# Kernel optimization log

Hardware: AMD Instinct MI355X
Metric: run time of the kernel (lower is better)

## Reference

```python
import jax, jax.numpy as jnp
import numpy as np

B, N, F_IN, ENC = 512, 512, 6, 128
EPS = 1e-5  # BatchNorm1d default eps


def _masked_bn_relu(h, m, gamma, beta):
    # h: [B,N,C]; m: [B,N,1] float mask. BN stats over valid points only,
    # matching torch's first_mlp(x[mask]) gather semantics (biased variance).
    cnt = jnp.maximum(m.sum(), 1.0)
    mean = (h * m).sum(axis=(0, 1)) / cnt
    var = (jnp.square(h - mean) * m).sum(axis=(0, 1)) / cnt
    hn = (h - mean) * jax.lax.rsqrt(var + EPS) * gamma + beta
    return jax.nn.relu(hn)


def setup_inputs() -> dict:
    key = jax.random.key(0)
    ks = jax.random.split(key, 16)
    s = lambda fan_in: 1.0 / np.sqrt(fan_in)
    inp = {
        "x": jax.random.normal(ks[0], (B, N, F_IN), dtype=jnp.float32),
        "mask": jax.random.bernoulli(ks[1], 0.7, (B, N)),
        # first_mlp: Linear(F_IN,128), BN(128), ReLU, Linear(128,256)
        "W1": jax.random.uniform(ks[2], (F_IN, 128), jnp.float32, -s(F_IN), s(F_IN)),
        "b1": jnp.zeros((128,), jnp.float32),
        "g1": jnp.ones((128,), jnp.float32),
        "be1": jnp.zeros((128,), jnp.float32),
        "W2": jax.random.uniform(ks[3], (128, 256), jnp.float32, -s(128), s(128)),
        "b2": jnp.zeros((256,), jnp.float32),
        # second_mlp: Linear(512,256), BN(256), ReLU, Linear(256,ENC)
        "W3": jax.random.uniform(ks[4], (512, 256), jnp.float32, -s(512), s(512)),
        "b3": jnp.zeros((256,), jnp.float32),
        "g2": jnp.ones((256,), jnp.float32),
        "be2": jnp.zeros((256,), jnp.float32),
        "W4": jax.random.uniform(ks[5], (256, ENC), jnp.float32, -s(256), s(256)),
        "b4": jnp.zeros((ENC,), jnp.float32),
    }
    return inp


def reference(x, mask, W1, b1, g1, be1, W2, b2, W3, b3, g2, be2, W4, b4):
    m = mask[..., None].astype(x.dtype)  # [B,N,1]
    # first_mlp on valid points; invalid positions become zeros (scatter into zeros buffer)
    h = x @ W1 + b1
    h = _masked_bn_relu(h, m, g1, be1)
    h = (h @ W2 + b2) * m  # [B,N,256], zeros where mask is False
    pooled = h.max(axis=1)  # [B,256] (zeros participate, as in torch)
    feat = jnp.concatenate(
        [h, jnp.broadcast_to(pooled[:, None, :], (h.shape[0], h.shape[1], pooled.shape[-1]))],
        axis=-1,
    )  # [B,N,512]
    h2 = feat @ W3 + b3
    h2 = _masked_bn_relu(h2, m, g2, be2)
    h2 = (h2 @ W4 + b4) * m  # [B,N,ENC], zeros where invalid
    return h2.max(axis=1)  # [B,ENC]
```

## Files before the change

kernel.cpp:

```cpp
#include <hip/hip_runtime.h>
#include <stdint.h>

#define BB   512
#define NN   512
#define MROWS (BB*NN)
#define RT   (MROWS/64)
#define EPSV 1e-5f

typedef unsigned short u16;
typedef __attribute__((ext_vector_type(8))) short bf16x8;
typedef __attribute__((ext_vector_type(4))) float f32x4;

__device__ __forceinline__ float read_mask(const void* mp, int r, int mode) {
  if (mode == 0) return ((const unsigned char*)mp)[r] ? 1.f : 0.f;
  if (mode == 1) return ((const unsigned int*)mp)[r] ? 1.f : 0.f;
  return ((const unsigned long long*)mp)[r] ? 1.f : 0.f;
}

__device__ __forceinline__ u16 f2bf(float f) {
  union { float f; unsigned int u; } v; v.f = f;
  unsigned int u = v.u;
  return (u16)((u + 0x7FFFu + ((u >> 16) & 1u)) >> 16);
}

__device__ __forceinline__ float bf2f(u16 b) {
  union { unsigned int u; float f; } t;
  t.u = ((unsigned int)b) << 16;
  return t.f;
}

__device__ __forceinline__ unsigned int cvt_pk_bf16(float lo, float hi) {
  unsigned int r;
  asm("v_cvt_pk_bf16_f32 %0, %1, %2" : "=v"(r) : "v"(lo), "v"(hi));
  return r;
}

__global__ __launch_bounds__(256) void k_prep(
    const float* __restrict__ W2, const float* __restrict__ W3, const float* __restrict__ W4,
    const float* __restrict__ b2, const unsigned char* __restrict__ mu,
    u16* __restrict__ w2t, u16* __restrict__ w4t,
    u16* __restrict__ w23t, float* __restrict__ c23, int* __restrict__ mode) {
  __shared__ float row[256];
  __shared__ int c1s, c4s;
  const int blk = blockIdx.x;
  if (blk < 256) {
    const int idx = blk*256 + threadIdx.x;
    if (idx < 32768) {
      const int n = idx >> 7, k = idx & 127;
      w2t[idx] = f2bf(W2[(size_t)k*256 + n]);
    } else {
      const int j = idx - 32768;
      const int n = j >> 8, k = j & 255;
      w4t[j] = f2bf(W4[(size_t)k*128 + n]);
    }
  } else if (blk < 385) {
    const int n = threadIdx.x;
    const int k = blk - 256;
    if (k < 128) {
      row[n] = W2[(size_t)k*256 + n];
      __syncthreads();
      float a0 = 0.f, a1 = 0.f, a2v = 0.f, a3 = 0.f;
      for (int j = 0; j < 256; j += 4) {
        a0 = fmaf(row[j  ], W3[(size_t)(j    )*256 + n], a0);
        a1 = fmaf(row[j+1], W3[(size_t)(j + 1)*256 + n], a1);
        a2v= fmaf(row[j+2], W3[(size_t)(j + 2)*256 + n], a2v);
        a3 = fmaf(row[j+3], W3[(size_t)(j + 3)*256 + n], a3);
      }
      w23t[(size_t)n*128 + k] = f2bf(((a0 + a1) + (a2v + a3)));
    } else {
      float a0 = 0.f, a1 = 0.f, a2v = 0.f, a3 = 0.f;
      for (int j = 0; j < 256; j += 4) {
        a0 = fmaf(b2[j  ], W3[(size_t)(j    )*256 + n], a0);
        a1 = fmaf(b2[j+1], W3[(size_t)(j + 1)*256 + n], a1);
        a2v= fmaf(b2[j+2], W3[(size_t)(j + 2)*256 + n], a2v);
        a3 = fmaf(b2[j+3], W3[(size_t)(j + 3)*256 + n], a3);
      }
      c23[n] = ((a0 + a1) + (a2v + a3));
    }
  } else {
    if (threadIdx.x == 0) { c1s = 0; c4s = 0; }
    __syncthreads();
    for (int i = threadIdx.x; i < 4096; i += 256) {
      const unsigned char b = mu[i];
      if (b) {
        if ((i & 3) == 1) atomicAdd(&c1s, 1);
        if ((i & 7) == 4) atomicAdd(&c4s, 1);
      }
    }
    __syncthreads();
    if (threadIdx.x == 0) *mode = c1s ? 0 : (c4s ? 1 : 2);
  }
}

__global__ __launch_bounds__(256) void k_stats1(
    const float* __restrict__ x, const void* __restrict__ mask,
    const int* __restrict__ modep,
    float* __restrict__ part, float* __restrict__ cntbf) {
  const int mode = *modep;
  const int tid = threadIdx.x;
  const int blk = blockIdx.x;
  float sx[6] = {0,0,0,0,0,0};
  float sxx[21] = {0};
  float cntq[4] = {0,0,0,0};
#pragma unroll
  for (int it = 0; it < 8; ++it) {
    const int r = blk*2048 + it*256 + tid;
    const float mv = read_mask(mask, r, mode);
    const float* xr = x + (size_t)r*6;
    const float2 p0 = *(const float2*)(xr);
    const float2 p1 = *(const float2*)(xr + 2);
    const float2 p2 = *(const float2*)(xr + 4);
    float v[6] = {p0.x, p0.y, p1.x, p1.y, p2.x, p2.y};
    cntq[it >> 1] += mv;
    int idx = 0;
#pragma unroll
    for (int j = 0; j < 6; ++j) {
      sx[j] = fmaf(mv, v[j], sx[j]);
      const float mj = mv * v[j];
#pragma unroll
      for (int k = j; k < 6; ++k) { sxx[idx] = fmaf(mj, v[k], sxx[idx]); ++idx; }
    }
  }
  float vals[32];
#pragma unroll
  for (int j = 0; j < 6; ++j) vals[j] = sx[j];
#pragma unroll
  for (int j = 0; j < 21; ++j) vals[6 + j] = sxx[j];
  vals[27] = 0.f;
#pragma unroll
  for (int q = 0; q < 4; ++q) vals[28 + q] = cntq[q];
#pragma unroll
  for (int j = 0; j < 32; ++j) {
#pragma unroll
    for (int m = 1; m <= 32; m <<= 1)
      vals[j] += __shfl_xor(vals[j], m, 64);
  }
  __shared__ float red[4][32];
  const int wave = tid >> 6, lane = tid & 63;
  if (lane == 0) {
#pragma unroll
    for (int j = 0; j < 32; ++j) red[wave][j] = vals[j];
  }
  __syncthreads();
  if (tid < 32) {
    const float tot = red[0][tid] + red[1][tid] + red[2][tid] + red[3][tid];
    part[(size_t)blk*32 + tid] = tot;
    if (tid >= 28) cntbf[blk*4 + (tid - 28)] = tot;
  }
}

__global__ __launch_bounds__(128) void k_fin1(
    const float* __restrict__ part,
    const float* __restrict__ W1, const float* __restrict__ b1,
    const float* __restrict__ g1, const float* __restrict__ be1,
    float* __restrict__ w1p, float* __restrict__ c1p, float* __restrict__ cntf) {
  __shared__ float tot[32];
  const int t = threadIdx.x;
  if (t < 32) {
    float a0 = 0.f, a1 = 0.f, a2v = 0.f, a3 = 0.f;
    for (int i = 0; i < 128; i += 4) {
      a0 += part[(size_t)(i    )*32 + t];
      a1 += part[(size_t)(i + 1)*32 + t];
      a2v+= part[(size_t)(i + 2)*32 + t];
      a3 += part[(size_t)(i + 3)*32 + t];
    }
    tot[t] = (a0 + a1) + (a2v + a3);
  }
  __syncthreads();
  float cnt = tot[28] + tot[29] + tot[30] + tot[31];
  if (cnt < 1.f) cnt = 1.f;
  if (t == 0) *cntf = cnt;
  const int c = t;
  float w[6];
#pragma unroll
  for (int k = 0; k < 6; ++k) w[k] = W1[k*128 + c];
  float s1 = 0.f;
#pragma unroll
  for (int k = 0; k < 6; ++k) s1 = fmaf(w[k], tot[k], s1);
  s1 /= cnt;
  float q = 0.f;
  {
    int idx = 6;
#pragma unroll
    for (int j = 0; j < 6; ++j) {
      q = fmaf(w[j]*w[j], tot[idx], q); ++idx;
#pragma unroll
      for (int k = j + 1; k < 6; ++k) { q = fmaf(2.f*w[j]*w[k], tot[idx], q); ++idx; }
    }
  }
  float var = q / cnt - s1*s1; if (var < 0.f) var = 0.f;
  const float mean = b1[c] + s1;
  const float a = g1[c] * rsqrtf(var + EPSV);
  const float sh = be1[c] - mean*a;
  c1p[c] = fmaf(b1[c], a, sh - b1[c]*a + (mean - s1)*0.f);
  c1p[c] = fmaf(b1[c], a, be1[c] - mean*a);
#pragma unroll
  for (int k = 0; k < 6; ++k) w1p[k*128 + c] = W1[k*128 + c] * a;
}

__global__ __launch_bounds__(256, 4) void k_mega(
    const float* __restrict__ x, const void* __restrict__ mask, const int* __restrict__ modep,
    const float* __restrict__ w1p, const float* __restrict__ c1p,
    const u16* __restrict__ W2t, const float* __restrict__ b2,
    const u16* __restrict__ W23t, const float* __restrict__ c23,
    u16* __restrict__ acc3buf, float* __restrict__ poolpart,
    float* __restrict__ s2sum, float* __restrict__ s2sq) {
  __shared__ u16 buf[64*264];
  __shared__ float xs[384];
  __shared__ float mk[64];
  const int mode = *modep;
  const int tid = threadIdx.x;
  const int rt = blockIdx.x;
  const int row0 = rt*64;
  const int b = rt >> 3, seg = rt & 7;
  for (int i = tid; i < 384; i += 256) xs[i] = x[(size_t)row0*6 + i];
  if (tid < 64) mk[tid] = read_mask(mask, row0 + tid, mode);
  __syncthreads();
  {
    const int c0 = (tid & 31) * 4;
    const int r0 = (tid >> 5) * 8;
    float4 wv[6];
#pragma unroll
    for (int k = 0; k < 6; ++k) wv[k] = *(const float4*)(w1p + k*128 + c0);
    const float4 cc = *(const float4*)(c1p + c0);
#pragma unroll
    for (int r = 0; r < 8; ++r) {
      const int row = r0 + r;
      float xv[6];
#pragma unroll
      for (int k = 0; k < 6; ++k) xv[k] = xs[row*6 + k];
      float v0 = cc.x, v1 = cc.y, v2 = cc.z, v3 = cc.w;
#pragma unroll
      for (int k = 0; k < 6; ++k) {
        v0 = fmaf(xv[k], wv[k].x, v0);
        v1 = fmaf(xv[k], wv[k].y, v1);
        v2 = fmaf(xv[k], wv[k].z, v2);
        v3 = fmaf(xv[k], wv[k].w, v3);
      }
      uint2 z;
      z.x = cvt_pk_bf16(fmaxf(v0, 0.f), fmaxf(v1, 0.f));
      z.y = cvt_pk_bf16(fmaxf(v2, 0.f), fmaxf(v3, 0.f));
      *(uint2*)(buf + row*136 + c0) = z;
    }
  }
  __syncthreads();
  const int wave = tid >> 6, lane = tid & 63;
  const int lr = lane & 15, lq = lane >> 4;
  {
    f32x4 acc[4][4];
#pragma unroll
    for (int r = 0; r < 4; ++r)
#pragma unroll
      for (int c = 0; c < 4; ++c) acc[r][c] = (f32x4){0.f,0.f,0.f,0.f};
#pragma unroll
    for (int kc = 0; kc < 128; kc += 32) {
      bf16x8 afr[4];
#pragma unroll
      for (int r = 0; r < 4; ++r)
        afr[r] = *(const bf16x8*)(buf + (r*16 + lr)*136 + kc + lq*8);
#pragma unroll
      for (int c = 0; c < 4; ++c) {
        const bf16x8 bfr = *(const bf16x8*)(W2t + (size_t)(wave*64 + c*16 + lr)*128 + kc + lq*8);
#pragma unroll
        for (int r = 0; r < 4; ++r)
          acc[r][c] = __builtin_amdgcn_mfma_f32_16x16x32_bf16(afr[r], bfr, acc[r][c], 0, 0, 0);
      }
    }
#pragma unroll
    for (int c = 0; c < 4; ++c) {
      const int col = wave*64 + c*16 + lr;
      const float bb = b2[col];
      float cm = -1e38f;
#pragma unroll
      for (int r = 0; r < 4; ++r) {
        const int base = r*16 + lq*4;
#pragma unroll
        for (int i = 0; i < 4; ++i)
          cm = fmaxf(cm, (acc[r][c][i] + bb) * mk[base + i]);
      }
      cm = fmaxf(cm, __shfl_xor(cm, 16, 64));
      cm = fmaxf(cm, __shfl_xor(cm, 32, 64));
      if (lq == 0) poolpart[((size_t)(b*8 + seg))*256 + col] = cm;
    }
  }
  f32x4 acc3[4][4];
#pragma unroll
  for (int r = 0; r < 4; ++r)
#pragma unroll
    for (int c = 0; c < 4; ++c) acc3[r][c] = (f32x4){0.f,0.f,0.f,0.f};
#pragma unroll
  for (int kc = 0; kc < 128; kc += 32) {
    bf16x8 afr[4];
#pragma unroll
    for (int r = 0; r < 4; ++r)
      afr[r] = *(const bf16x8*)(buf + (r*16 + lr)*136 + kc + lq*8);
#pragma unroll
    for (int c = 0; c < 4; ++c) {
      const bf16x8 bfr = *(const bf16x8*)(W23t + (size_t)(wave*64 + c*16 + lr)*128 + kc + lq*8);
#pragma unroll
      for (int r = 0; r < 4; ++r)
        acc3[r][c] = __builtin_amdgcn_mfma_f32_16x16x32_bf16(afr[r], bfr, acc3[r][c], 0, 0, 0);
    }
  }
  __syncthreads();
#pragma unroll
  for (int c = 0; c < 4; ++c) {
    const int col = wave*64 + c*16 + lr;
    const float cc3 = c23[col];
    float sS = 0.f, sQ = 0.f;
#pragma unroll
    for (int r = 0; r < 4; ++r) {
      const int base = r*16 + lq*4;
#pragma unroll
      for (int i = 0; i < 4; i += 2) {
        const float a0 = (acc3[r][c][i]   + cc3) * mk[base + i];
        const float a1 = (acc3[r][c][i+1] + cc3) * mk[base + i + 1];
        const unsigned int u = cvt_pk_bf16(a0, a1);
        buf[(base + i    )*264 + col] = (u16)u;
        buf[(base + i + 1)*264 + col] = (u16)(u >> 16);
        sS += a0 + a1;
        sQ += a0*a0 + a1*a1;
      }
    }
    sS += __shfl_xor(sS, 16, 64);
    sS += __shfl_xor(sS, 32, 64);
    sQ += __shfl_xor(sQ, 16, 64);
    sQ += __shfl_xor(sQ, 32, 64);
    if (lq == 0) {
      s2sum[(size_t)rt*256 + col] = sS;
      s2sq [(size_t)rt*256 + col] = sQ;
    }
  }
  __syncthreads();
  for (int it = tid; it < 64*32; it += 256) {
    const int row = it >> 5, c8 = it & 31;
    *(uint4*)(acc3buf + (size_t)(row0 + row)*256 + c8*8) = *(const uint4*)(buf + row*264 + c8*8);
  }
}

__global__ __launch_bounds__(256) void k_poolP(
    const float* __restrict__ poolpart, const float* __restrict__ W3,
    const float* __restrict__ b3, float* __restrict__ P) {
  __shared__ float pl[256];
  const int b = blockIdx.x, tid = threadIdx.x;
  float m = poolpart[((size_t)b*8)*256 + tid];
#pragma unroll
  for (int s = 1; s < 8; ++s) m = fmaxf(m, poolpart[((size_t)(b*8+s))*256 + tid]);
  pl[tid] = m;
  __syncthreads();
  float a0 = 0.f, a1 = 0.f, a2v = 0.f, a3 = 0.f;
  for (int c = 0; c < 256; c += 4) {
    a0 = fmaf(pl[c  ], W3[(size_t)(256 + c    )*256 + tid], a0);
    a1 = fmaf(pl[c+1], W3[(size_t)(256 + c + 1)*256 + tid], a1);
    a2v= fmaf(pl[c+2], W3[(size_t)(256 + c + 2)*256 + tid], a2v);
    a3 = fmaf(pl[c+3], W3[(size_t)(256 + c + 3)*256 + tid], a3);
  }
  P[(size_t)b*256 + tid] = ((a0 + a1) + (a2v + a3)) + b3[tid];
}

__global__ __launch_bounds__(256) void k_red2(
    const float* __restrict__ s2sum, const float* __restrict__ s2sq,
    const float* __restrict__ cntbf, const float* __restrict__ P,
    float* __restrict__ midS, float* __restrict__ midQ) {
  const int slab = blockIdx.x;
  const int c = threadIdx.x;
  float accS = 0.f, accQ = 0.f;
  for (int b = slab*8; b < slab*8 + 8; ++b) {
    const float cntb = cntbf[b];
    float S = 0.f, Q = 0.f;
#pragma unroll
    for (int s = 0; s < 8; ++s) {
      S += s2sum[(size_t)(b*8 + s)*256 + c];
      Q += s2sq [(size_t)(b*8 + s)*256 + c];
    }
    const float p = P[(size_t)b*256 + c];
    accS += fmaf(cntb, p, S);
    accQ += fmaf(cntb, p*p, fmaf(2.f*p, S, Q));
  }
  midS[slab*256 + c] = accS;
  midQ[slab*256 + c] = accQ;
}

__global__ __launch_bounds__(256) void k_fin2(
    const float* __restrict__ midS, const float* __restrict__ midQ,
    const float* __restrict__ cntf,
    const float* __restrict__ g2, const float* __restrict__ be2,
    float* __restrict__ a2, float* __restrict__ sh2) {
  const int c = threadIdx.x;
  float s = 0.f, q = 0.f;
#pragma unroll 8
  for (int k = 0; k < 64; ++k) { s += midS[k*256 + c]; q += midQ[k*256 + c]; }
  const float cf = *cntf;
  const float mean = s / cf;
  float var = q / cf - mean*mean; if (var < 0.f) var = 0.f;
  const float a = g2[c] * rsqrtf(var + EPSV);
  a2[c]  = a;
  sh2[c] = be2[c] - mean*a;
}

__global__ __launch_bounds__(512, 4) void k_gemm4(
    const u16* __restrict__ acc3buf, const void* __restrict__ mask, const int* __restrict__ modep,
    const float* __restrict__ P, const float* __restrict__ a2, const float* __restrict__ sh2,
    const u16* __restrict__ W4t, const float* __restrict__ b4,
    float* __restrict__ out) {
  __shared__ u16 a2t[64*264];
  __shared__ float a2l[256], s2b[256];
  __shared__ float mk[64];
  const int mode = *modep;
  const int tid = threadIdx.x;
  const int b = blockIdx.x;
  const int wave = tid >> 6, lane = tid & 63;
  const int lr = lane & 15, lq = lane >> 4;
  const size_t rowbase = (size_t)b*512;
  if (tid < 256) {
    const float aa = a2[tid];
    a2l[tid] = aa;
    s2b[tid] = fmaf(P[(size_t)b*256 + tid], aa, sh2[tid]);
  }
  bf16x8 bw[8];
#pragma unroll
  for (int j = 0; j < 8; ++j)
    bw[j] = *(const bf16x8*)(W4t + (size_t)(wave*16 + lr)*256 + j*32 + lq*8);
  const float bb = b4[wave*16 + lr];
  float cm = -1e38f;
  uint4 u[4];
#pragma unroll
  for (int it = 0; it < 4; ++it) {
    const int j = tid + it*512;
    u[it] = *(const uint4*)(acc3buf + (rowbase + (j >> 5))*256 + (j & 31)*8);
  }
  for (int seg = 0; seg < 8; ++seg) {
    __syncthreads();
#pragma unroll
    for (int it = 0; it < 4; ++it) {
      const int j = tid + it*512;
      const int row = j >> 5, c8 = j & 31;
      const u16* us = (const u16*)&u[it];
      unsigned int pk[4];
#pragma unroll
      for (int jj = 0; jj < 4; ++jj) {
        const int cc0 = c8*8 + jj*2, cc1 = cc0 + 1;
        const float z0 = fmaf(bf2f(us[jj*2    ]), a2l[cc0], s2b[cc0]);
        const float z1 = fmaf(bf2f(us[jj*2 + 1]), a2l[cc1], s2b[cc1]);
        pk[jj] = cvt_pk_bf16(fmaxf(z0, 0.f), fmaxf(z1, 0.f));
      }
      *(uint4*)(a2t + row*264 + c8*8) = *(const uint4*)pk;
    }
    if (tid < 64) mk[tid] = read_mask(mask, (int)(rowbase + seg*64 + tid), mode);
    if (seg < 7) {
#pragma unroll
      for (int it = 0; it < 4; ++it) {
        const int j = tid + it*512;
        u[it] = *(const uint4*)(acc3buf + (rowbase + (seg + 1)*64 + (j >> 5))*256 + (j & 31)*8);
      }
    }
    __syncthreads();
    f32x4 acc[4];
#pragma unroll
    for (int r = 0; r < 4; ++r) acc[r] = (f32x4){0.f,0.f,0.f,0.f};
#pragma unroll
    for (int kc8 = 0; kc8 < 8; ++kc8) {
      bf16x8 afr[4];
#pragma unroll
      for (int r = 0; r < 4; ++r)
        afr[r] = *(const bf16x8*)(a2t + (r*16 + lr)*264 + kc8*32 + lq*8);
#pragma unroll
      for (int r = 0; r < 4; ++r)
        acc[r] = __builtin_amdgcn_mfma_f32_16x16x32_bf16(afr[r], bw[kc8], acc[r], 0, 0, 0);
    }
#pragma unroll
    for (int r = 0; r < 4; ++r) {
#pragma unroll
      for (int i = 0; i < 4; ++i)
        cm = fmaxf(cm, (acc[r][i] + bb) * mk[r*16 + lq*4 + i]);
    }
  }
  cm = fmaxf(cm, __shfl_xor(cm, 16, 64));
  cm = fmaxf(cm, __shfl_xor(cm, 32, 64));
  if (lq == 0) out[(size_t)b*128 + wave*16 + lr] = cm;
}

extern "C" void kernel_launch(void* const* d_in, const int* in_sizes, int n_in,
                              void* d_out, int out_size, void* d_ws, size_t ws_size,
                              hipStream_t stream) {
  const float* x    = (const float*)d_in[0];
  const void*  mask = d_in[1];
  const float* W1   = (const float*)d_in[2];
  const float* b1   = (const float*)d_in[3];
  const float* g1   = (const float*)d_in[4];
  const float* be1  = (const float*)d_in[5];
  const float* W2   = (const float*)d_in[6];
  const float* b2   = (const float*)d_in[7];
  const float* W3   = (const float*)d_in[8];
  const float* b3   = (const float*)d_in[9];
  const float* g2   = (const float*)d_in[10];
  const float* be2  = (const float*)d_in[11];
  const float* W4   = (const float*)d_in[12];
  const float* b4   = (const float*)d_in[13];
  float* out = (float*)d_out;

  char* ws = (char*)d_ws;
  size_t off = 0;
  auto take = [&](size_t bytes) -> char* {
    char* p = ws + off;
    off = (off + bytes + 255) & ~(size_t)255;
    return p;
  };
  u16*   acc3buf = (u16*)  take((size_t)MROWS*256*2);
  float* part    = (float*)take((size_t)128*32*4);
  float* cntbf   = (float*)take((size_t)512*4);
  float* w1p     = (float*)take(768*4);
  float* c1p     = (float*)take(128*4);
  float* cntf    = (float*)take(256);
  float* poolpart= (float*)take((size_t)512*8*256*4);
  float* P       = (float*)take((size_t)512*256*4);
  float* s2sum   = (float*)take((size_t)RT*256*4);
  float* s2sq    = (float*)take((size_t)RT*256*4);
  float* midS    = (float*)take((size_t)64*256*4);
  float* midQ    = (float*)take((size_t)64*256*4);
  float* a2      = (float*)take(256*4);
  float* sh2     = (float*)take(256*4);
  int*   modep   = (int*)  take(256);
  u16*   w2t     = (u16*)  take((size_t)256*128*2);
  u16*   w23t    = (u16*)  take((size_t)256*128*2);
  u16*   w4t     = (u16*)  take((size_t)128*256*2);
  float* c23     = (float*)take(256*4);

  k_prep<<<386, 256, 0, stream>>>(W2, W3, W4, b2, (const unsigned char*)mask,
                                  w2t, w4t, w23t, c23, modep);
  k_stats1<<<128, 256, 0, stream>>>(x, mask, modep, part, cntbf);
  k_fin1<<<1, 128, 0, stream>>>(part, W1, b1, g1, be1, w1p, c1p, cntf);
  k_mega<<<RT, 256, 0, stream>>>(x, mask, modep, w1p, c1p, w2t, b2, w23t, c23,
                                 acc3buf, poolpart, s2sum, s2sq);
  k_poolP<<<512, 256, 0, stream>>>(poolpart, W3, b3, P);
  k_red2<<<64, 256, 0, stream>>>(s2sum, s2sq, cntbf, P, midS, midQ);
  k_fin2<<<1, 256, 0, stream>>>(midS, midQ, cntf, g2, be2, a2, sh2);
  k_gemm4<<<512, 512, 0, stream>>>(acc3buf, mask, modep, P, a2, sh2, w4t, b4, out);
}
```

Before: 242.8 us.

## Fuse pooled projection, BN2 stat reduction and finalize into one kernel

Merges k_poolP, k_red2 and k_fin2 into a single k_pool2 kernel with 512 threads per block. The pooled-vector GEMV is split across two halves of the block, and per-batch statistics are accumulated into global sums with float atomics. The last block to finish, found through an atomic counter, computes the BN scale and shift. This removes two kernel launches and the intermediate midS/midQ slabs, at the cost of atomic contention on 256 addresses and a nondeterministic float summation order.

```diff
diff --git a/kernel.cpp b/kernel.cpp
--- a/kernel.cpp
+++ b/kernel.cpp
@@ -39,7 +39,8 @@
     const float* __restrict__ W2, const float* __restrict__ W3, const float* __restrict__ W4,
     const float* __restrict__ b2, const unsigned char* __restrict__ mu,
     u16* __restrict__ w2t, u16* __restrict__ w4t,
-    u16* __restrict__ w23t, float* __restrict__ c23, int* __restrict__ mode) {
+    u16* __restrict__ w23t, float* __restrict__ c23, int* __restrict__ mode,
+    float* __restrict__ midS, float* __restrict__ midQ, int* __restrict__ ctr) {
   __shared__ float row[256];
   __shared__ int c1s, c4s;
   const int blk = blockIdx.x;
@@ -78,6 +79,9 @@
       c23[n] = ((a0 + a1) + (a2v + a3));
     }
   } else {
+    midS[threadIdx.x] = 0.f;
+    midQ[threadIdx.x] = 0.f;
+    if (threadIdx.x == 0) *ctr = 0;
     if (threadIdx.x == 0) { c1s = 0; c4s = 0; }
     __syncthreads();
     for (int i = threadIdx.x; i < 4096; i += 256) {
@@ -191,8 +195,6 @@
   float var = q / cnt - s1*s1; if (var < 0.f) var = 0.f;
   const float mean = b1[c] + s1;
   const float a = g1[c] * rsqrtf(var + EPSV);
-  const float sh = be1[c] - mean*a;
-  c1p[c] = fmaf(b1[c], a, sh - b1[c]*a + (mean - s1)*0.f);
   c1p[c] = fmaf(b1[c], a, be1[c] - mean*a);
 #pragma unroll
   for (int k = 0; k < 6; ++k) w1p[k*128 + c] = W1[k*128 + c] * a;
@@ -338,64 +340,65 @@
   }
 }
 
-__global__ __launch_bounds__(256) void k_poolP(
+__global__ __launch_bounds__(512) void k_pool2(
     const float* __restrict__ poolpart, const float* __restrict__ W3,
-    const float* __restrict__ b3, float* __restrict__ P) {
+    const float* __restrict__ b3,
+    const float* __restrict__ s2sum, const float* __restrict__ s2sq,
+    const float* __restrict__ cntbf, const float* __restrict__ cntf,
+    const float* __restrict__ g2, const float* __restrict__ be2,
+    float* __restrict__ P, float* __restrict__ midS, float* __restrict__ midQ,
+    float* __restrict__ a2, float* __restrict__ sh2, int* __restrict__ ctr) {
   __shared__ float pl[256];
+  __shared__ float part2[2][256];
+  __shared__ int lastdone;
   const int b = blockIdx.x, tid = threadIdx.x;
-  float m = poolpart[((size_t)b*8)*256 + tid];
-#pragma unroll
-  for (int s = 1; s < 8; ++s) m = fmaxf(m, poolpart[((size_t)(b*8+s))*256 + tid]);
-  pl[tid] = m;
-  __syncthreads();
-  float a0 = 0.f, a1 = 0.f, a2v = 0.f, a3 = 0.f;
-  for (int c = 0; c < 256; c += 4) {
-    a0 = fmaf(pl[c  ], W3[(size_t)(256 + c    )*256 + tid], a0);
-    a1 = fmaf(pl[c+1], W3[(size_t)(256 + c + 1)*256 + tid], a1);
-    a2v= fmaf(pl[c+2], W3[(size_t)(256 + c + 2)*256 + tid], a2v);
-    a3 = fmaf(pl[c+3], W3[(size_t)(256 + c + 3)*256 + tid], a3);
-  }
-  P[(size_t)b*256 + tid] = ((a0 + a1) + (a2v + a3)) + b3[tid];
-}
-
-__global__ __launch_bounds__(256) void k_red2(
-    const float* __restrict__ s2sum, const float* __restrict__ s2sq,
-    const float* __restrict__ cntbf, const float* __restrict__ P,
-    float* __restrict__ midS, float* __restrict__ midQ) {
-  const int slab = blockIdx.x;
-  const int c = threadIdx.x;
-  float accS = 0.f, accQ = 0.f;
-  for (int b = slab*8; b < slab*8 + 8; ++b) {
+  if (tid < 256) {
+    float m = poolpart[((size_t)b*8)*256 + tid];
+#pragma unroll
+    for (int s = 1; s < 8; ++s) m = fmaxf(m, poolpart[((size_t)(b*8+s))*256 + tid]);
+    pl[tid] = m;
+  }
+  __syncthreads();
+  {
+    const int col = tid & 255, half = tid >> 8;
+    const int cbase = half*128;
+    float a0 = 0.f, a1 = 0.f, a2v = 0.f, a3 = 0.f;
+    for (int c = cbase; c < cbase + 128; c += 4) {
+      a0 = fmaf(pl[c  ], W3[(size_t)(256 + c    )*256 + col], a0);
+      a1 = fmaf(pl[c+1], W3[(size_t)(256 + c + 1)*256 + col], a1);
+      a2v= fmaf(pl[c+2], W3[(size_t)(256 + c + 2)*256 + col], a2v);
+      a3 = fmaf(pl[c+3], W3[(size_t)(256 + c + 3)*256 + col], a3);
+    }
+    part2[half][col] = (a0 + a1) + (a2v + a3);
+  }
+  __syncthreads();
+  if (tid < 256) {
+    const float p = part2[0][tid] + part2[1][tid] + b3[tid];
+    P[(size_t)b*256 + tid] = p;
+    float S = 0.f, Q = 0.f;
+#pragma unroll
+    for (int s = 0; s < 8; ++s) {
+      S += s2sum[(size_t)(b*8 + s)*256 + tid];
+      Q += s2sq [(size_t)(b*8 + s)*256 + tid];
+    }
     const float cntb = cntbf[b];
-    float S = 0.f, Q = 0.f;
-#pragma unroll
-    for (int s = 0; s < 8; ++s) {
-      S += s2sum[(size_t)(b*8 + s)*256 + c];
-      Q += s2sq [(size_t)(b*8 + s)*256 + c];
-    }
-    const float p = P[(size_t)b*256 + c];
-    accS += fmaf(cntb, p, S);
-    accQ += fmaf(cntb, p*p, fmaf(2.f*p, S, Q));
-  }
-  midS[slab*256 + c] = accS;
-  midQ[slab*256 + c] = accQ;
-}
-
-__global__ __launch_bounds__(256) void k_fin2(
-    const float* __restrict__ midS, const float* __restrict__ midQ,
-    const float* __restrict__ cntf,
-    const float* __restrict__ g2, const float* __restrict__ be2,
-    float* __restrict__ a2, float* __restrict__ sh2) {
-  const int c = threadIdx.x;
-  float s = 0.f, q = 0.f;
-#pragma unroll 8
-  for (int k = 0; k < 64; ++k) { s += midS[k*256 + c]; q += midQ[k*256 + c]; }
-  const float cf = *cntf;
-  const float mean = s / cf;
-  float var = q / cf - mean*mean; if (var < 0.f) var = 0.f;
-  const float a = g2[c] * rsqrtf(var + EPSV);
-  a2[c]  = a;
-  sh2[c] = be2[c] - mean*a;
+    atomicAdd(&midS[tid], fmaf(cntb, p, S));
+    atomicAdd(&midQ[tid], fmaf(cntb, p*p, fmaf(2.f*p, S, Q)));
+  }
+  __threadfence();
+  __syncthreads();
+  if (tid == 0) lastdone = atomicAdd(ctr, 1);
+  __syncthreads();
+  if (lastdone == 511 && tid < 256) {
+    const float s = atomicAdd(&midS[tid], 0.f);
+    const float q = atomicAdd(&midQ[tid], 0.f);
+    const float cf = *cntf;
+    const float mean = s / cf;
+    float var = q / cf - mean*mean; if (var < 0.f) var = 0.f;
+    const float a = g2[tid] * rsqrtf(var + EPSV);
+    a2[tid]  = a;
+    sh2[tid] = be2[tid] - mean*a;
+  }
 }
 
 __global__ __launch_bounds__(512, 4) void k_gemm4(
@@ -516,24 +519,24 @@
   float* P       = (float*)take((size_t)512*256*4);
   float* s2sum   = (float*)take((size_t)RT*256*4);
   float* s2sq    = (float*)take((size_t)RT*256*4);
-  float* midS    = (float*)take((size_t)64*256*4);
-  float* midQ    = (float*)take((size_t)64*256*4);
+  float* midS    = (float*)take((size_t)256*4);
+  float* midQ    = (float*)take((size_t)256*4);
   float* a2      = (float*)take(256*4);
   float* sh2     = (float*)take(256*4);
   int*   modep   = (int*)  take(256);
+  int*   ctr     = (int*)  take(256);
   u16*   w2t     = (u16*)  take((size_t)256*128*2);
   u16*   w23t    = (u16*)  take((size_t)256*128*2);
   u16*   w4t     = (u16*)  take((size_t)128*256*2);
   float* c23     = (float*)take(256*4);
 
   k_prep<<<386, 256, 0, stream>>>(W2, W3, W4, b2, (const unsigned char*)mask,
-                                  w2t, w4t, w23t, c23, modep);
+                                  w2t, w4t, w23t, c23, modep, midS, midQ, ctr);
   k_stats1<<<128, 256, 0, stream>>>(x, mask, modep, part, cntbf);
   k_fin1<<<1, 128, 0, stream>>>(part, W1, b1, g1, be1, w1p, c1p, cntf);
   k_mega<<<RT, 256, 0, stream>>>(x, mask, modep, w1p, c1p, w2t, b2, w23t, c23,
                                  acc3buf, poolpart, s2sum, s2sq);
-  k_poolP<<<512, 256, 0, stream>>>(poolpart, W3, b3, P);
-  k_red2<<<64, 256, 0, stream>>>(s2sum, s2sq, cntbf, P, midS, midQ);
-  k_fin2<<<1, 256, 0, stream>>>(midS, midQ, cntf, g2, be2, a2, sh2);
+  k_pool2<<<512, 512, 0, stream>>>(poolpart, W3, b3, s2sum, s2sq, cntbf, cntf,
+                                   g2, be2, P, midS, midQ, a2, sh2, ctr);
   k_gemm4<<<512, 512, 0, stream>>>(acc3buf, mask, modep, P, a2, sh2, w4t, b4, out);
 }
```

Result: slower. 303.4 us (+25.0%).
